# Performance work log

Measured on AMD Instinct MI355X. Metric: run time of the kernel, lower is better.

The kernel has to match this reference:

```python
import jax, jax.numpy as jnp
import numpy as np

BN_EPS = 1e-5

def _conv1x1(x, w, b=None):
    # x: [B,C,H,W], w: [O,C] -> [B,O,H,W]
    y = jnp.einsum('bchw,oc->bohw', x, w)
    if b is not None:
        y = y + b[None, :, None, None]
    return y

def _bn_silu(y, gamma, beta):
    # BN inference with running_mean=0, running_var=1, then SiLU
    scale = gamma / jnp.sqrt(1.0 + BN_EPS)
    y = y * scale[None, :, None, None] + beta[None, :, None, None]
    return jax.nn.silu(y)

def setup_inputs() -> dict:
    key = jax.random.key(0)
    ks = jax.random.split(key, 20)
    B, D, S = 32, 512, 32
    C = D // 2
    d = {}
    d['x'] = jax.random.normal(ks[0], (B, D, S, S), jnp.float32)
    d['cv1_w'] = jax.random.normal(ks[1], (C, D), jnp.float32) * (1.0 / np.sqrt(D))
    d['cv1_gamma'] = jax.random.uniform(ks[2], (C,), jnp.float32, 0.5, 1.5)
    d['cv1_beta'] = jax.random.normal(ks[3], (C,), jnp.float32) * 0.1
    d['q_w'] = jax.random.normal(ks[4], (C, C), jnp.float32) * (1.0 / np.sqrt(C))
    d['q_b'] = jax.random.normal(ks[5], (C,), jnp.float32) * 0.02
    d['k_w'] = jax.random.normal(ks[6], (C, C), jnp.float32) * (1.0 / np.sqrt(C))
    d['k_b'] = jax.random.normal(ks[7], (C,), jnp.float32) * 0.02
    d['v_w'] = jax.random.normal(ks[8], (C, C), jnp.float32) * (1.0 / np.sqrt(C))
    d['v_b'] = jax.random.normal(ks[9], (C,), jnp.float32) * 0.02
    d['e_w'] = jax.random.normal(ks[10], (C, C), jnp.float32) * (1.0 / np.sqrt(C))
    d['e_b'] = jax.random.normal(ks[11], (C,), jnp.float32) * 0.02
    d['rel_h'] = jax.random.normal(ks[12], (1, C, S, 1), jnp.float32)
    d['rel_w'] = jax.random.normal(ks[13], (1, C, 1, S), jnp.float32)
    d['cv2_w'] = jax.random.normal(ks[14], (D, C), jnp.float32) * (1.0 / np.sqrt(C))
    d['cv2_gamma'] = jax.random.uniform(ks[15], (D,), jnp.float32, 0.5, 1.5)
    d['cv2_beta'] = jax.random.normal(ks[16], (D,), jnp.float32) * 0.1
    return d

def reference(x, cv1_w, cv1_gamma, cv1_beta, q_w, q_b, k_w, k_b, v_w, v_b,
              e_w, e_b, rel_h, rel_w, cv2_w, cv2_gamma, cv2_beta):
    # cv1: 1x1 conv (no bias) + BN + SiLU
    x1 = _bn_silu(_conv1x1(x, cv1_w), cv1_gamma, cv1_beta)  # [B,C,H,W]
    B, C, H, W = x1.shape
    N = H * W
    q = _conv1x1(x1, q_w, q_b).reshape(B, C, N)
    k = _conv1x1(x1, k_w, k_b).reshape(B, C, N)
    v = _conv1x1(x1, v_w, v_b).reshape(B, C, N)
    e = _conv1x1(x1, e_w, e_b).reshape(B, C, N)
    # content-content: q^T k -> [B,N,N]
    cc = jnp.einsum('bci,bcj->bij', q, k)
    # content-position: (rel_h + rel_w) flattened to [C,N], times extra proj
    pos = (rel_h + rel_w).reshape(C, N)  # broadcast add -> [1,C,H,W] -> [C,N]
    cp = jnp.einsum('ci,bcj->bij', pos, e)  # [B,N,N]
    attn = jax.nn.softmax(cc + cp, axis=-1)
    # out[b,c,i] = sum_j v[b,c,j] * attn[b,i,j]
    out = jnp.einsum('bcj,bij->bci', v, attn).reshape(B, C, H, W)
    y = _bn_silu(_conv1x1(out, cv2_w), cv2_gamma, cv2_beta)
    return x + y
```

## Files before the change

kernel.cpp:

```cpp
#include <hip/hip_runtime.h>
#include <hip/hip_bf16.h>

typedef unsigned short u16;
typedef __attribute__((ext_vector_type(8))) _Float16 half8;
typedef __attribute__((ext_vector_type(4))) float f32x4;

__device__ __forceinline__ u16 f2h(float f) {
  _Float16 h = (_Float16)f;
  union { _Float16 h; u16 u; } a; a.h = h;
  return a.u;
}

__device__ __forceinline__ float h2f(u16 u) {
  union { _Float16 h; u16 u; } a; a.u = u;
  return (float)a.h;
}

__device__ __forceinline__ float silu_f(float y) {
  return y / (1.0f + __expf(-y));
}

__device__ __forceinline__ void glds16(const u16* g, u16* l) {
  __builtin_amdgcn_global_load_lds(
      (__attribute__((address_space(1))) unsigned*)(g),
      (__attribute__((address_space(3))) unsigned*)(l), 16, 0, 0);
}

enum { EPI_BNSILU_N = 0, EPI_QKEV, EPI_RAW_F16, EPI_BNSILU_RES_M };

template<int EPI, bool DUAL, int TILES, int GX>
__global__ __launch_bounds__(256, 2)
void gemm_nt(const u16* __restrict__ A, long long a_bs, int lda,
             const u16* __restrict__ A2,
             const u16* __restrict__ B, long long b_bs, int ldb,
             void* __restrict__ C0, long long c_bs, int ldc,
             void* __restrict__ C1, void* __restrict__ C2,
             int K,
             const float* __restrict__ p0, const float* __restrict__ p1,
             const float* __restrict__ res, long long res_bs)
{
  __shared__ u16 smem[32768];

  const int id = blockIdx.x;
  const int bz = (id & 7) + 8 * (id / (8 * TILES));
  const int tt = (id >> 3) % TILES;
  const int bm = tt % GX;
  const int bn = tt / GX;
  const u16* Ab = A + (long long)bz * a_bs;
  const u16* Bb = B + (long long)bz * b_bs;
  const int m0 = bm * 128;
  const int n0 = bn * 128;
  const int t = threadIdx.x;
  const int lane = t & 63;
  const int w = t >> 6;
  const int wm = (w & 1) * 64;
  const int wn = (w >> 1) * 64;
  const int q = lane >> 4;
  const int lr = lane & 15;

  f32x4 acc[4][4];
#pragma unroll
  for (int i = 0; i < 4; ++i)
#pragma unroll
    for (int j = 0; j < 4; ++j)
      acc[i][j] = (f32x4){0.f, 0.f, 0.f, 0.f};

  const int lrow = lane >> 2;
  const int kch = (lane & 3) ^ ((lane >> 2) & 3) ^ ((lane >> 4) & 3);
  const int lk = kch * 8;
  const u16* aR0 = Ab + (long long)(m0 + 32 * w + lrow) * lda + lk;
  const u16* aR1 = aR0 + 16LL * lda;
  const u16* bR0 = Bb + (long long)(n0 + 32 * w + lrow) * ldb + lk;
  const u16* bR1 = bR0 + 16LL * ldb;
  const u16* a2R0 = nullptr; const u16* a2R1 = nullptr;
  if constexpr (DUAL) {
    a2R0 = A2 + (long long)(m0 + 32 * w + lrow) * 256 + lk;
    a2R1 = a2R0 + 16LL * 256;
  }
  u16* la0 = smem + w * 1024;         u16* la1 = la0 + 512;
  u16* lb0 = smem + 16384 + w * 1024; u16* lb1 = lb0 + 512;
  const int fpos = (q ^ (lr & 3) ^ ((lr >> 2) & 3)) * 8;

  for (int k0 = 0; k0 < K; k0 += 128) {
    __syncthreads();
    if (!DUAL || k0 < 256) {
#pragma unroll
      for (int s = 0; s < 4; ++s) {
        const int ko = k0 + 32 * s;
        glds16(aR0 + ko, la0 + s * 4096);
        glds16(aR1 + ko, la1 + s * 4096);
      }
    } else {
#pragma unroll
      for (int s = 0; s < 4; ++s) {
        const int ko = k0 - 256 + 32 * s;
        glds16(a2R0 + ko, la0 + s * 4096);
        glds16(a2R1 + ko, la1 + s * 4096);
      }
    }
#pragma unroll
    for (int s = 0; s < 4; ++s) {
      const int ko = k0 + 32 * s;
      glds16(bR0 + ko, lb0 + s * 4096);
      glds16(bR1 + ko, lb1 + s * 4096);
    }
    __syncthreads();
#pragma unroll
    for (int h = 0; h < 4; ++h) {
      half8 af[4], bfr[4];
#pragma unroll
      for (int i = 0; i < 4; ++i)
        af[i] = *(const half8*)&smem[h * 4096 + (wm + i * 16 + lr) * 32 + fpos];
#pragma unroll
      for (int j = 0; j < 4; ++j)
        bfr[j] = *(const half8*)&smem[16384 + h * 4096 + (wn + j * 16 + lr) * 32 + fpos];
#pragma unroll
      for (int i = 0; i < 4; ++i)
#pragma unroll
        for (int j = 0; j < 4; ++j)
          acc[i][j] = __builtin_amdgcn_mfma_f32_16x16x32_f16(af[i], bfr[j], acc[i][j], 0, 0, 0);
    }
  }

  if constexpr (EPI == EPI_BNSILU_N) {
    u16* Cg = (u16*)C0 + (long long)bz * c_bs;
#pragma unroll
    for (int i = 0; i < 4; ++i)
#pragma unroll
      for (int j = 0; j < 4; ++j)
#pragma unroll
        for (int r = 0; r < 4; ++r) {
          const int m = m0 + wm + i * 16 + q * 4 + r;
          const int n = n0 + wn + j * 16 + lr;
          float v = acc[i][j][r];
          v = silu_f(v * (p0[n] * 0.99999500003749969f) + p1[n]);
          Cg[(long long)m * ldc + n] = f2h(v);
        }
  } else if constexpr (EPI == EPI_RAW_F16) {
    u16* Cg = (u16*)C0 + (long long)bz * c_bs;
#pragma unroll
    for (int i = 0; i < 4; ++i)
#pragma unroll
      for (int j = 0; j < 4; ++j)
#pragma unroll
        for (int r = 0; r < 4; ++r) {
          const int m = m0 + wm + i * 16 + q * 4 + r;
          const int n = n0 + wn + j * 16 + lr;
          Cg[(long long)m * ldc + n] = f2h(acc[i][j][r]);
        }
  } else if constexpr (EPI == EPI_BNSILU_RES_M) {
    float* Cg = (float*)C0 + (long long)bz * c_bs;
    const float* rg = res + (long long)bz * res_bs;
#pragma unroll
    for (int i = 0; i < 4; ++i)
#pragma unroll
      for (int j = 0; j < 4; ++j)
#pragma unroll
        for (int r = 0; r < 4; ++r) {
          const int m = m0 + wm + i * 16 + q * 4 + r;
          const int n = n0 + wn + j * 16 + lr;
          float v = acc[i][j][r];
          v = silu_f(v * (p0[m] * 0.99999500003749969f) + p1[m]);
          const long long idx = (long long)m * ldc + n;
          Cg[idx] = v + rg[idx];
        }
  } else {
    const int seg = n0 >> 8;
    const int nb = n0 & 255;
    if (seg < 3) {
      u16* dst; long long bs; int ld2;
      if (seg == 0) { dst = (u16*)C0; bs = 262144; ld2 = 256; }
      else { dst = (u16*)C1 + (seg == 2 ? 256 : 0); bs = 524288; ld2 = 512; }
      dst += (long long)bz * bs;
#pragma unroll
      for (int i = 0; i < 4; ++i)
#pragma unroll
        for (int j = 0; j < 4; ++j)
#pragma unroll
          for (int r = 0; r < 4; ++r) {
            const int m = m0 + wm + i * 16 + q * 4 + r;
            const int col = wn + j * 16 + lr;
            float v = acc[i][j][r] + p0[n0 + col];
            dst[(long long)m * ld2 + nb + col] = f2h(v);
          }
    } else {
      u16* dst = (u16*)C2 + (long long)bz * 262144;
#pragma unroll
      for (int s = 0; s < 4; ++s) {
        const int rbase = s * 32;
        __syncthreads();
        if (wm == (rbase & 64)) {
          const int ibase = (rbase & 32) >> 4;
#pragma unroll
          for (int ii = 0; ii < 2; ++ii) {
            const int i = ibase + ii;
#pragma unroll
            for (int j = 0; j < 4; ++j)
#pragma unroll
              for (int r = 0; r < 4; ++r) {
                const int row32 = i * 16 + q * 4 + r - (rbase & 32);
                const int col = wn + j * 16 + lr;
                float v = acc[i][j][r] + p0[768 + nb + col];
                smem[row32 * 132 + col] = f2h(v);
              }
          }
        }
        __syncthreads();
#pragma unroll
        for (int p = 0; p < 2; ++p) {
          const int lin = p * 256 + t;
          const int c = lin >> 2;
          const int mc = lin & 3;
          u16 tmp[8];
#pragma unroll
          for (int r8 = 0; r8 < 8; ++r8)
            tmp[r8] = smem[(mc * 8 + r8) * 132 + c];
          *(half8*)&dst[(long long)(nb + c) * 1024 + m0 + rbase + mc * 8] =
              *(const half8*)tmp;
        }
      }
    }
  }
}

__global__ __launch_bounds__(256)
void transpose_x(const float* __restrict__ x, u16* __restrict__ xT) {
  __shared__ float tile[64][65];
  const int b = blockIdx.z;
  const int n0 = blockIdx.x * 64;
  const int d0 = blockIdx.y * 64;
  const int t = threadIdx.x;
  const float* src = x + (long long)b * 524288;
  const int rr = t >> 4;
  const int cc = t & 15;
#pragma unroll
  for (int i = 0; i < 4; ++i) {
    const int r = rr + i * 16;
    const float4 v = *(const float4*)&src[(long long)(d0 + r) * 1024 + n0 + cc * 4];
    tile[r][cc * 4 + 0] = v.x;
    tile[r][cc * 4 + 1] = v.y;
    tile[r][cc * 4 + 2] = v.z;
    tile[r][cc * 4 + 3] = v.w;
  }
  __syncthreads();
  u16* dst = xT + (long long)b * 524288;
  const int d8 = t & 7;
  const int nn = t >> 3;
#pragma unroll
  for (int i = 0; i < 2; ++i) {
    const int n = nn + i * 32;
    u16 tmp[8];
#pragma unroll
    for (int e = 0; e < 8; ++e) tmp[e] = f2h(tile[d8 * 8 + e][n]);
    *(half8*)&dst[(long long)(n0 + n) * 512 + d0 + d8 * 8] = *(const half8*)tmp;
  }
}

__global__ __launch_bounds__(256)
void convert_w(const float* __restrict__ w1, const float* __restrict__ wq,
               const float* __restrict__ wk, const float* __restrict__ wv,
               const float* __restrict__ we, const float* __restrict__ w2,
               const float* __restrict__ bq, const float* __restrict__ bk,
               const float* __restrict__ be, const float* __restrict__ bv,
               u16* __restrict__ dstw, float* __restrict__ bbuf) {
  int id = blockIdx.x * 256 + threadIdx.x;
  if (id < 524288) {
    float v;
    if (id < 131072) v = w1[id];
    else if (id < 393216) {
      int s = id - 131072, o = s >> 8, c = s & 255;
      if (o < 256) v = wq[o * 256 + c];
      else if (o < 512) v = wk[(o - 256) * 256 + c];
      else if (o < 768) v = we[(o - 512) * 256 + c];
      else v = wv[(o - 768) * 256 + c];
    } else v = w2[id - 393216];
    dstw[id] = f2h(v);
  } else {
    int i = id - 524288;
    float v;
    if (i < 256) v = bq[i];
    else if (i < 512) v = bk[i - 256];
    else if (i < 768) v = be[i - 512];
    else v = bv[i - 768];
    bbuf[i] = v;
  }
}

__global__ __launch_bounds__(256)
void pos_compute(const float* __restrict__ rh, const float* __restrict__ rw,
                 u16* __restrict__ posT) {
  const int n = blockIdx.x;
  const int c = threadIdx.x;
  posT[n * 256 + c] = f2h(rh[c * 32 + (n >> 5)] + rw[c * 32 + (n & 31)]);
}

__global__ __launch_bounds__(256)
void softmax_rows(u16* __restrict__ logits) {
  __shared__ float redm[2][2], reds[2][2];
  const int t = threadIdx.x;
  const int row = t >> 7;
  const int l = t & 127;
  const int wv = (t >> 6) & 1;
  u16* p = logits + (long long)blockIdx.x * 2048 + row * 1024;
  half8 raw = ((const half8*)p)[l];
  float v[8];
#pragma unroll
  for (int e = 0; e < 8; ++e) v[e] = (float)raw[e];
  float mx = v[0];
#pragma unroll
  for (int e = 1; e < 8; ++e) mx = fmaxf(mx, v[e]);
#pragma unroll
  for (int off = 32; off > 0; off >>= 1) mx = fmaxf(mx, __shfl_down(mx, off));
  if ((t & 63) == 0) redm[row][wv] = mx;
  __syncthreads();
  mx = fmaxf(redm[row][0], redm[row][1]);
  float ev[8];
  float s = 0.f;
#pragma unroll
  for (int e = 0; e < 8; ++e) { ev[e] = __expf(v[e] - mx); s += ev[e]; }
#pragma unroll
  for (int off = 32; off > 0; off >>= 1) s += __shfl_down(s, off);
  if ((t & 63) == 0) reds[row][wv] = s;
  __syncthreads();
  const float inv = 1.0f / (reds[row][0] + reds[row][1]);
  half8 o;
#pragma unroll
  for (int e = 0; e < 8; ++e) o[e] = (_Float16)(ev[e] * inv);
  ((half8*)p)[l] = o;
}

extern "C" void kernel_launch(void* const* d_in, const int* in_sizes, int n_in,
                              void* d_out, int out_size, void* d_ws, size_t ws_size,
                              hipStream_t stream) {
  const float* x  = (const float*)d_in[0];
  const float* w1 = (const float*)d_in[1];
  const float* g1 = (const float*)d_in[2];
  const float* b1 = (const float*)d_in[3];
  const float* wq = (const float*)d_in[4];
  const float* bq = (const float*)d_in[5];
  const float* wk = (const float*)d_in[6];
  const float* bk = (const float*)d_in[7];
  const float* wv = (const float*)d_in[8];
  const float* bv = (const float*)d_in[9];
  const float* we = (const float*)d_in[10];
  const float* be = (const float*)d_in[11];
  const float* rh = (const float*)d_in[12];
  const float* rw = (const float*)d_in[13];
  const float* w2 = (const float*)d_in[14];
  const float* g2 = (const float*)d_in[15];
  const float* b2 = (const float*)d_in[16];
  float* out = (float*)d_out;
  char* ws = (char*)d_ws;

  u16* xT     = (u16*)(ws + 0);
  u16* x1t    = (u16*)(ws + 33554432);
  u16* qbuf   = (u16*)(ws + 50331648);
  u16* kcat   = (u16*)(ws + 67108864);
  u16* vbuf   = (u16*)(ws + 100663296);
  u16* outt   = (u16*)(ws + 117440512);
  u16* posT   = (u16*)(ws + 134217728);
  u16* wbuf   = (u16*)(ws + 134742016);
  float* bbuf = (float*)(ws + 135790592);
  u16* logits = (u16*)(ws + 142606336);

  u16* w1b    = wbuf;
  u16* wqkve  = wbuf + 131072;
  u16* w2b    = wbuf + 393216;

  transpose_x<<<dim3(16, 8, 32), 256, 0, stream>>>(x, xT);
  convert_w<<<dim3(2052), 256, 0, stream>>>(w1, wq, wk, wv, we, w2,
                                            bq, bk, be, bv, wbuf, bbuf);
  pos_compute<<<dim3(1024), 256, 0, stream>>>(rh, rw, posT);

  gemm_nt<EPI_BNSILU_N, false, 16, 8><<<dim3(512), 256, 0, stream>>>(
      xT, 524288LL, 512, nullptr, w1b, 0LL, 512,
      x1t, 262144LL, 256, nullptr, nullptr, 512, g1, b1, nullptr, 0LL);

  gemm_nt<EPI_QKEV, false, 64, 8><<<dim3(2048), 256, 0, stream>>>(
      x1t, 262144LL, 256, nullptr, wqkve, 0LL, 256,
      qbuf, 262144LL, 256, kcat, vbuf, 256, bbuf, nullptr, nullptr, 0LL);

  gemm_nt<EPI_RAW_F16, true, 64, 8><<<dim3(2048), 256, 0, stream>>>(
      qbuf, 262144LL, 256, posT, kcat, 524288LL, 512,
      logits, 1048576LL, 1024, nullptr, nullptr, 512, nullptr, nullptr, nullptr, 0LL);

  softmax_rows<<<dim3(16384), 256, 0, stream>>>(logits);

  gemm_nt<EPI_RAW_F16, false, 16, 8><<<dim3(512), 256, 0, stream>>>(
      logits, 1048576LL, 1024, nullptr, vbuf, 262144LL, 1024,
      outt, 262144LL, 256, nullptr, nullptr, 1024, nullptr, nullptr, nullptr, 0LL);

  gemm_nt<EPI_BNSILU_RES_M, false, 32, 4><<<dim3(1024), 256, 0, stream>>>(
      w2b, 0LL, 256, nullptr, outt, 262144LL, 256,
      out, 524288LL, 1024, nullptr, nullptr, 256, g2, b2, x, 524288LL);
}
```

Baseline: 326.9 us.

## Add 256x256-tile 512-thread MFMA GEMM for attention logits

Adds a dedicated GEMM kernel with 256x256 output tiles, 8 waves per block, XOR-swizzled LDS layout and direct global-to-LDS loads. It computes the concatenated q/pos times k/e logits product. Larger tiles raise arithmetic intensity and cut redundant operand reloads relative to the generic 64-tile kernel. The trade-offs are a large accumulator register footprint per thread, fewer blocks (512), no double buffering, and scattered scalar f16 stores in the epilogue.

After: 327.1 us. Within noise of the previous version (+0.1%).

```diff
diff --git a/kernel.cpp b/kernel.cpp
--- a/kernel.cpp
+++ b/kernel.cpp
@@ -221,6 +221,94 @@
       }
     }
   }
+}
+
+template<bool DUAL>
+__global__ __launch_bounds__(512, 2)
+void gemm256_nt(const u16* __restrict__ A, long long a_bs, int lda,
+                const u16* __restrict__ A2,
+                const u16* __restrict__ B, long long b_bs, int ldb,
+                u16* __restrict__ C0, long long c_bs, int ldc, int K)
+{
+  __shared__ u16 smem[32768];
+
+  const int id = blockIdx.x;
+  const int bz = (id & 7) + 8 * (id / (8 * 16));
+  const int tt = (id >> 3) % 16;
+  const int m0 = (tt & 3) * 256;
+  const int n0 = (tt >> 2) * 256;
+  const u16* Ab = A + (long long)bz * a_bs;
+  const u16* Bb = B + (long long)bz * b_bs;
+  const int t = threadIdx.x;
+  const int lane = t & 63;
+  const int w = t >> 6;
+  const int wm = (w & 1) * 128;
+  const int wn = (w >> 1) * 64;
+  const int q = lane >> 4;
+  const int lr = lane & 15;
+
+  f32x4 acc[8][4];
+#pragma unroll
+  for (int i = 0; i < 8; ++i)
+#pragma unroll
+    for (int j = 0; j < 4; ++j)
+      acc[i][j] = (f32x4){0.f, 0.f, 0.f, 0.f};
+
+  const int lrow = lane >> 2;
+  const int kch = (lane & 3) ^ ((lane >> 2) & 3) ^ ((lane >> 4) & 3);
+  const int lk = kch * 8;
+  const u16* aR0 = Ab + (long long)(m0 + 32 * w + lrow) * lda + lk;
+  const u16* aR1 = aR0 + 16LL * lda;
+  const u16* bR0 = Bb + (long long)(n0 + 32 * w + lrow) * ldb + lk;
+  const u16* bR1 = bR0 + 16LL * ldb;
+  const u16* a2R0 = nullptr; const u16* a2R1 = nullptr;
+  if constexpr (DUAL) {
+    a2R0 = A2 + (long long)(m0 + 32 * w + lrow) * 256 + lk;
+    a2R1 = a2R0 + 16LL * 256;
+  }
+  u16* la0 = smem + w * 1024;         u16* la1 = la0 + 512;
+  u16* lb0 = smem + 16384 + w * 1024; u16* lb1 = lb0 + 512;
+  const int fpos = (q ^ (lr & 3) ^ ((lr >> 2) & 3)) * 8;
+
+  for (int k0 = 0; k0 < K; k0 += 64) {
+    __syncthreads();
+    if (!DUAL || k0 < 256) {
+      glds16(aR0 + k0, la0);        glds16(aR1 + k0, la1);
+      glds16(aR0 + k0 + 32, la0 + 8192); glds16(aR1 + k0 + 32, la1 + 8192);
+    } else {
+      glds16(a2R0 + (k0 - 256), la0);        glds16(a2R1 + (k0 - 256), la1);
+      glds16(a2R0 + (k0 - 224), la0 + 8192); glds16(a2R1 + (k0 - 224), la1 + 8192);
+    }
+    glds16(bR0 + k0, lb0);        glds16(bR1 + k0, lb1);
+    glds16(bR0 + k0 + 32, lb0 + 8192); glds16(bR1 + k0 + 32, lb1 + 8192);
+    __syncthreads();
+#pragma unroll
+    for (int h = 0; h < 2; ++h) {
+      half8 bfr[4];
+#pragma unroll
+      for (int j = 0; j < 4; ++j)
+        bfr[j] = *(const half8*)&smem[16384 + h * 8192 + (wn + j * 16 + lr) * 32 + fpos];
+#pragma unroll
+      for (int i = 0; i < 8; ++i) {
+        const half8 af = *(const half8*)&smem[h * 8192 + (wm + i * 16 + lr) * 32 + fpos];
+#pragma unroll
+        for (int j = 0; j < 4; ++j)
+          acc[i][j] = __builtin_amdgcn_mfma_f32_16x16x32_f16(af, bfr[j], acc[i][j], 0, 0, 0);
+      }
+    }
+  }
+
+  u16* Cg = C0 + (long long)bz * c_bs;
+#pragma unroll
+  for (int i = 0; i < 8; ++i)
+#pragma unroll
+    for (int j = 0; j < 4; ++j)
+#pragma unroll
+      for (int r = 0; r < 4; ++r) {
+        const int m = m0 + wm + i * 16 + q * 4 + r;
+        const int n = n0 + wn + j * 16 + lr;
+        Cg[(long long)m * ldc + n] = f2h(acc[i][j][r]);
+      }
 }
 
 __global__ __launch_bounds__(256)
@@ -380,9 +468,9 @@
       x1t, 262144LL, 256, nullptr, wqkve, 0LL, 256,
       qbuf, 262144LL, 256, kcat, vbuf, 256, bbuf, nullptr, nullptr, 0LL);
 
-  gemm_nt<EPI_RAW_F16, true, 64, 8><<<dim3(2048), 256, 0, stream>>>(
+  gemm256_nt<true><<<dim3(512), 512, 0, stream>>>(
       qbuf, 262144LL, 256, posT, kcat, 524288LL, 512,
-      logits, 1048576LL, 1024, nullptr, nullptr, 512, nullptr, nullptr, nullptr, 0LL);
+      logits, 1048576LL, 1024, 512);
 
   softmax_rows<<<dim3(16384), 256, 0, stream>>>(logits);
 
```
